# Performance work log

Measured on AMD Instinct MI355X. Metric: run time of the kernel, lower is better.

Reference implementation:

```python
import jax, jax.numpy as jnp
import numpy as np

NODE_DIM = 32
EDGE_DIM = 16
N_A = 1024
N_B = 1024
EDGE_IN = 2 * NODE_DIM + 2 * EDGE_DIM   # 96
NODE_IN = NODE_DIM + EDGE_DIM           # 48


def _linear_init(key, fan_in, fan_out):
    # torch nn.Linear default init: U(-1/sqrt(fan_in), 1/sqrt(fan_in))
    kw, kb = jax.random.split(key)
    bound = 1.0 / np.sqrt(fan_in)
    W = jax.random.uniform(kw, (fan_in, fan_out), jnp.float32, -bound, bound)
    b = jax.random.uniform(kb, (fan_out,), jnp.float32, -bound, bound)
    return W, b


def setup_inputs() -> dict:
    key = jax.random.key(0)
    ks = jax.random.split(key, 7)
    edge_embeds = jax.random.normal(ks[0], (N_A, N_B, 2 * EDGE_DIM), jnp.float32)
    nodes_a_embeds = jax.random.normal(ks[1], (N_A, NODE_DIM), jnp.float32)
    nodes_b_embeds = jax.random.normal(ks[2], (N_B, NODE_DIM), jnp.float32)
    We1, be1 = _linear_init(ks[3], EDGE_IN, EDGE_DIM)
    We2, be2 = _linear_init(ks[4], EDGE_DIM, EDGE_DIM)
    Wn1, bn1 = _linear_init(ks[5], NODE_IN, NODE_DIM)
    Wn2, bn2 = _linear_init(ks[6], NODE_DIM, NODE_DIM)
    return {
        "edge_embeds": edge_embeds,
        "nodes_a_embeds": nodes_a_embeds,
        "nodes_b_embeds": nodes_b_embeds,
        "We1": We1, "be1": be1, "We2": We2, "be2": be2,
        "Wn1": Wn1, "bn1": bn1, "Wn2": Wn2, "bn2": bn2,
    }


def _edge_mlp(x, We1, be1, We2, be2):
    h = jax.nn.relu(x @ We1 + be1)
    return jax.nn.relu(h @ We2 + be2)


def _node_mlp(x, Wn1, bn1, Wn2, bn2):
    h = jax.nn.relu(x @ Wn1 + bn1)
    return jax.nn.relu(h @ Wn2 + bn2)


def reference(edge_embeds, nodes_a_embeds, nodes_b_embeds,
              We1, be1, We2, be2, Wn1, bn1, Wn2, bn2):
    nA, nB, _ = edge_embeds.shape
    # edge update: broadcast node feats over the bipartite grid, concat, 2-layer MLP
    a_bcast = jnp.broadcast_to(nodes_a_embeds[:, None, :], (nA, nB, NODE_DIM))
    b_bcast = jnp.broadcast_to(nodes_b_embeds[None, :, :], (nA, nB, NODE_DIM))
    edge_in = jnp.concatenate([a_bcast, b_bcast, edge_embeds], axis=-1)  # (A,B,96)
    new_edges = _edge_mlp(edge_in, We1, be1, We2, be2)                   # (A,B,E)
    # node update: sum-aggregate messages, concat with node feats, 2-layer MLP
    msg_to_a = new_edges.sum(axis=1)  # (A,E)
    msg_to_b = new_edges.sum(axis=0)  # (B,E)
    new_a = _node_mlp(jnp.concatenate([nodes_a_embeds, msg_to_a], axis=-1), Wn1, bn1, Wn2, bn2)
    new_b = _node_mlp(jnp.concatenate([nodes_b_embeds, msg_to_b], axis=-1), Wn1, bn1, Wn2, bn2)
    return (new_edges, new_a, new_b)
```

## Files before the change

kernel.cpp:

```cpp
#include <hip/hip_runtime.h>
#include <hip/hip_bf16.h>

typedef float f32x4 __attribute__((ext_vector_type(4)));
typedef short s16x8 __attribute__((ext_vector_type(8)));

__device__ __forceinline__ unsigned short f2bf(float x) {
  return __bfloat16_as_ushort(__float2bfloat16(x));
}

__global__ void preab_kernel(const float* __restrict__ na, const float* __restrict__ nb,
                             const float* __restrict__ We1, const float* __restrict__ be1,
                             float* __restrict__ preA, float* __restrict__ preB) {
  int tid = blockIdx.x * blockDim.x + threadIdx.x;
  bool isB = tid >= 1024;
  int row = tid & 1023;
  const float* x = (isB ? nb : na) + row * 32;
  const float* W = We1 + (isB ? 32 * 16 : 0);
  float acc[16];
#pragma unroll
  for (int k = 0; k < 16; ++k) acc[k] = isB ? be1[k] : 0.f;
#pragma unroll
  for (int v = 0; v < 32; ++v) {
    float xv = x[v];
#pragma unroll
    for (int k = 0; k < 16; ++k) acc[k] += xv * W[v * 16 + k];
  }
  float* dst = (isB ? preB : preA) + row * 16;
#pragma unroll
  for (int q = 0; q < 4; ++q) {
    f32x4 o = {acc[q * 4], acc[q * 4 + 1], acc[q * 4 + 2], acc[q * 4 + 3]};
    *(f32x4*)&dst[q * 4] = o;
  }
}

__global__ __launch_bounds__(256, 4)
void edge_kernel(const float* __restrict__ E,
                 const float* __restrict__ We1,
                 const float* __restrict__ We2,
                 const float* __restrict__ be2,
                 const float* __restrict__ preA_g,
                 const float* __restrict__ preB_g,
                 float* __restrict__ outE,
                 float* __restrict__ msgA,
                 float* __restrict__ msgB) {
  __shared__ float sA[32 * 16];
  __shared__ float sB[32 * 20];
  __shared__ float sCS[4 * 512];

  const int t = threadIdx.x;
  const int bi = blockIdx.y, bj = blockIdx.x;

  if (t < 128) {
    int r = t >> 2, q = (t & 3) << 2;
    *(f32x4*)&sA[r * 16 + q] = *(const f32x4*)&preA_g[(bi * 32 + r) * 16 + q];
  } else {
    int tt = t - 128, r = tt >> 2, q = (tt & 3) << 2;
    *(f32x4*)&sB[r * 20 + q] = *(const f32x4*)&preB_g[(bj * 32 + r) * 16 + q];
  }

  const int w = t >> 6, lane = t & 63, G = lane >> 4, n = lane & 15;

  s16x8 a1, a2;
#pragma unroll
  for (int i2 = 0; i2 < 8; ++i2) {
    int k = G * 8 + i2;
    a1[i2] = (short)f2bf(We1[(64 + k) * 16 + n]);
    a2[i2] = (k < 16) ? (short)f2bf(We2[k * 16 + n]) : (short)0;
  }
  const f32x4 bq = *(const f32x4*)&be2[G * 4];

  __syncthreads();

  f32x4 cs0 = {0.f, 0.f, 0.f, 0.f}, cs1 = {0.f, 0.f, 0.f, 0.f};
  const f32x4 zero = {0.f, 0.f, 0.f, 0.f};

  for (int ii = 0; ii < 8; ++ii) {
    const int iloc = w * 8 + ii;
    const int i = bi * 32 + iloc;
    const f32x4 pA = *(const f32x4*)&sA[iloc * 16 + G * 4];
    f32x4 rs = {0.f, 0.f, 0.f, 0.f};
#pragma unroll
    for (int jg = 0; jg < 2; ++jg) {
      const int j = bj * 32 + jg * 16 + n;
      const float* ep = E + ((long)(i * 1024 + j) << 5) + G * 8;
      f32x4 e0 = __builtin_nontemporal_load((const f32x4*)ep);
      f32x4 e1 = __builtin_nontemporal_load((const f32x4*)(ep + 4));
      s16x8 bf;
      bf[0] = (short)f2bf(e0[0]); bf[1] = (short)f2bf(e0[1]);
      bf[2] = (short)f2bf(e0[2]); bf[3] = (short)f2bf(e0[3]);
      bf[4] = (short)f2bf(e1[0]); bf[5] = (short)f2bf(e1[1]);
      bf[6] = (short)f2bf(e1[2]); bf[7] = (short)f2bf(e1[3]);
      f32x4 d1 = __builtin_amdgcn_mfma_f32_16x16x32_bf16(a1, bf, zero, 0, 0, 0);
      const f32x4 pB = *(const f32x4*)&sB[(jg * 16 + n) * 20 + G * 4];
      float h0 = fmaxf(d1[0] + pA[0] + pB[0], 0.f);
      float h1 = fmaxf(d1[1] + pA[1] + pB[1], 0.f);
      float h2 = fmaxf(d1[2] + pA[2] + pB[2], 0.f);
      float h3 = fmaxf(d1[3] + pA[3] + pB[3], 0.f);
      unsigned p0 = (unsigned)f2bf(h0) | ((unsigned)f2bf(h1) << 16);
      unsigned p1 = (unsigned)f2bf(h2) | ((unsigned)f2bf(h3) << 16);
      int s0 = G * 32 + n;
      unsigned u0 = (unsigned)__shfl((int)p0, s0);
      unsigned u1 = (unsigned)__shfl((int)p1, s0);
      unsigned u2 = (unsigned)__shfl((int)p0, s0 + 16);
      unsigned u3 = (unsigned)__shfl((int)p1, s0 + 16);
      union { s16x8 v; unsigned u[4]; } b2;
      b2.u[0] = u0; b2.u[1] = u1; b2.u[2] = u2; b2.u[3] = u3;
      f32x4 d2 = __builtin_amdgcn_mfma_f32_16x16x32_bf16(a2, b2.v, zero, 0, 0, 0);
      f32x4 o;
      o[0] = fmaxf(d2[0] + bq[0], 0.f);
      o[1] = fmaxf(d2[1] + bq[1], 0.f);
      o[2] = fmaxf(d2[2] + bq[2], 0.f);
      o[3] = fmaxf(d2[3] + bq[3], 0.f);
      __builtin_nontemporal_store(o, (f32x4*)&outE[((long)(i * 1024 + j) << 4) + G * 4]);
      rs += o;
      if (jg == 0) cs0 += o; else cs1 += o;
    }
#pragma unroll
    for (int mask = 1; mask < 16; mask <<= 1) {
      rs[0] += __shfl_xor(rs[0], mask);
      rs[1] += __shfl_xor(rs[1], mask);
      rs[2] += __shfl_xor(rs[2], mask);
      rs[3] += __shfl_xor(rs[3], mask);
    }
    if (n < 4) {
      float val = (n == 0) ? rs[0] : (n == 1) ? rs[1] : (n == 2) ? rs[2] : rs[3];
      atomicAdd(&msgA[i * 16 + G * 4 + n], val);
    }
  }
  *(f32x4*)&sCS[w * 512 + n * 16 + G * 4] = cs0;
  *(f32x4*)&sCS[w * 512 + 256 + n * 16 + G * 4] = cs1;
  __syncthreads();
#pragma unroll
  for (int rep = 0; rep < 2; ++rep) {
    int idx = t + rep * 256;
    float s = sCS[idx] + sCS[512 + idx] + sCS[1024 + idx] + sCS[1536 + idx];
    int jg = idx >> 8, jl = (idx >> 4) & 15, c = idx & 15;
    atomicAdd(&msgB[(bj * 32 + jg * 16 + jl) * 16 + c], s);
  }
}

__global__ void node_kernel(const float* __restrict__ na, const float* __restrict__ nb,
                            const float* __restrict__ msgA, const float* __restrict__ msgB,
                            const float* __restrict__ Wn1, const float* __restrict__ bn1,
                            const float* __restrict__ Wn2, const float* __restrict__ bn2,
                            float* __restrict__ outA, float* __restrict__ outB) {
  int tid = blockIdx.x * blockDim.x + threadIdx.x;
  bool isB = tid >= 1024;
  int row = tid & 1023;
  const float* x0 = (isB ? nb : na) + row * 32;
  const float* m0 = (isB ? msgB : msgA) + row * 16;
  float h[32];
#pragma unroll
  for (int m = 0; m < 32; ++m) h[m] = bn1[m];
#pragma unroll 4
  for (int v = 0; v < 32; ++v) {
    float xv = x0[v];
#pragma unroll
    for (int m = 0; m < 32; ++m) h[m] += xv * Wn1[v * 32 + m];
  }
#pragma unroll 4
  for (int v = 0; v < 16; ++v) {
    float mv = m0[v];
#pragma unroll
    for (int m = 0; m < 32; ++m) h[m] += mv * Wn1[(32 + v) * 32 + m];
  }
#pragma unroll
  for (int m = 0; m < 32; ++m) h[m] = fmaxf(h[m], 0.f);
  float* dst = (isB ? outB : outA) + row * 32;
#pragma unroll 4
  for (int c = 0; c < 32; ++c) {
    float s = bn2[c];
#pragma unroll
    for (int m = 0; m < 32; ++m) s += h[m] * Wn2[m * 32 + c];
    dst[c] = fmaxf(s, 0.f);
  }
}

extern "C" void kernel_launch(void* const* d_in, const int* in_sizes, int n_in,
                              void* d_out, int out_size, void* d_ws, size_t ws_size,
                              hipStream_t stream) {
  const float* E   = (const float*)d_in[0];
  const float* na  = (const float*)d_in[1];
  const float* nb  = (const float*)d_in[2];
  const float* We1 = (const float*)d_in[3];
  const float* be1 = (const float*)d_in[4];
  const float* We2 = (const float*)d_in[5];
  const float* be2 = (const float*)d_in[6];
  const float* Wn1 = (const float*)d_in[7];
  const float* bn1 = (const float*)d_in[8];
  const float* Wn2 = (const float*)d_in[9];
  const float* bn2 = (const float*)d_in[10];

  float* out  = (float*)d_out;
  float* outE = out;
  float* outA = out + 16777216;
  float* outB = outA + 32768;

  float* ws   = (float*)d_ws;
  float* preA = ws;
  float* preB = ws + 16384;
  float* msgA = ws + 32768;
  float* msgB = ws + 49152;

  hipMemsetAsync(msgA, 0, 2 * 16384 * sizeof(float), stream);
  preab_kernel<<<dim3(8), dim3(256), 0, stream>>>(na, nb, We1, be1, preA, preB);
  edge_kernel<<<dim3(32, 32), dim3(256), 0, stream>>>(E, We1, We2, be2, preA, preB,
                                                      outE, msgA, msgB);
  node_kernel<<<dim3(8), dim3(256), 0, stream>>>(na, nb, msgA, msgB,
                                                 Wn1, bn1, Wn2, bn2, outA, outB);
}
```

Before: 261.7 us.

## Fuse node pre-projection into edge kernel and replace atomics with partial-sum buffers

Folds the separate pre-projection kernel into the edge kernel, where each block computes its own 32-row A/B projections. Global atomics for the message sums are replaced by per-block partial writes that the node kernel reduces, which also removes the memset. The second edge layer now uses a 16x16x16 MFMA with no cross-lane shuffles, and the edge loads for both column groups are issued up front. In exchange, each block recomputes small projections, and the node kernel must read 32 partials per row.

```diff
diff --git a/kernel.cpp b/kernel.cpp
--- a/kernel.cpp
+++ b/kernel.cpp
@@ -3,46 +3,33 @@
 
 typedef float f32x4 __attribute__((ext_vector_type(4)));
 typedef short s16x8 __attribute__((ext_vector_type(8)));
+typedef short s16x4 __attribute__((ext_vector_type(4)));
 
 __device__ __forceinline__ unsigned short f2bf(float x) {
   return __bfloat16_as_ushort(__float2bfloat16(x));
 }
 
-__global__ void preab_kernel(const float* __restrict__ na, const float* __restrict__ nb,
-                             const float* __restrict__ We1, const float* __restrict__ be1,
-                             float* __restrict__ preA, float* __restrict__ preB) {
-  int tid = blockIdx.x * blockDim.x + threadIdx.x;
-  bool isB = tid >= 1024;
-  int row = tid & 1023;
-  const float* x = (isB ? nb : na) + row * 32;
-  const float* W = We1 + (isB ? 32 * 16 : 0);
-  float acc[16];
-#pragma unroll
-  for (int k = 0; k < 16; ++k) acc[k] = isB ? be1[k] : 0.f;
-#pragma unroll
-  for (int v = 0; v < 32; ++v) {
-    float xv = x[v];
-#pragma unroll
-    for (int k = 0; k < 16; ++k) acc[k] += xv * W[v * 16 + k];
-  }
-  float* dst = (isB ? preB : preA) + row * 16;
-#pragma unroll
-  for (int q = 0; q < 4; ++q) {
-    f32x4 o = {acc[q * 4], acc[q * 4 + 1], acc[q * 4 + 2], acc[q * 4 + 3]};
-    *(f32x4*)&dst[q * 4] = o;
-  }
+__device__ __forceinline__ f32x4 mfma16x16x16_bf16(s16x4 a, s16x4 b, f32x4 c) {
+#if __has_builtin(__builtin_amdgcn_mfma_f32_16x16x16bf16_1k)
+  return __builtin_amdgcn_mfma_f32_16x16x16bf16_1k(a, b, c, 0, 0, 0);
+#else
+  f32x4 d;
+  asm("v_mfma_f32_16x16x16_bf16 %0, %1, %2, %3" : "=v"(d) : "v"(a), "v"(b), "v"(c));
+  return d;
+#endif
 }
 
 __global__ __launch_bounds__(256, 4)
 void edge_kernel(const float* __restrict__ E,
+                 const float* __restrict__ na,
+                 const float* __restrict__ nb,
                  const float* __restrict__ We1,
+                 const float* __restrict__ be1,
                  const float* __restrict__ We2,
                  const float* __restrict__ be2,
-                 const float* __restrict__ preA_g,
-                 const float* __restrict__ preB_g,
                  float* __restrict__ outE,
-                 float* __restrict__ msgA,
-                 float* __restrict__ msgB) {
+                 float* __restrict__ rowP,
+                 float* __restrict__ colP) {
   __shared__ float sA[32 * 16];
   __shared__ float sB[32 * 20];
   __shared__ float sCS[4 * 512];
@@ -50,62 +37,73 @@
   const int t = threadIdx.x;
   const int bi = blockIdx.y, bj = blockIdx.x;
 
-  if (t < 128) {
-    int r = t >> 2, q = (t & 3) << 2;
-    *(f32x4*)&sA[r * 16 + q] = *(const f32x4*)&preA_g[(bi * 32 + r) * 16 + q];
-  } else {
-    int tt = t - 128, r = tt >> 2, q = (tt & 3) << 2;
-    *(f32x4*)&sB[r * 20 + q] = *(const f32x4*)&preB_g[(bj * 32 + r) * 16 + q];
+  {
+    const bool half = t >= 128;
+    const int tt = t & 127, r = tt >> 2, qs = (tt & 3) << 2;
+    const float* x = (half ? nb : na) + (half ? bj : bi) * 32 * 32 + r * 32;
+    const float* W = We1 + (half ? 32 * 16 : 0) + qs;
+    f32x4 acc;
+    if (half) acc = *(const f32x4*)&be1[qs];
+    else { acc[0] = acc[1] = acc[2] = acc[3] = 0.f; }
+#pragma unroll 8
+    for (int v = 0; v < 32; ++v) {
+      float xv = x[v];
+      f32x4 wv = *(const f32x4*)&W[v * 16];
+      acc[0] += xv * wv[0]; acc[1] += xv * wv[1];
+      acc[2] += xv * wv[2]; acc[3] += xv * wv[3];
+    }
+    if (half) *(f32x4*)&sB[r * 20 + qs] = acc;
+    else      *(f32x4*)&sA[r * 16 + qs] = acc;
   }
 
   const int w = t >> 6, lane = t & 63, G = lane >> 4, n = lane & 15;
 
-  s16x8 a1, a2;
-#pragma unroll
-  for (int i2 = 0; i2 < 8; ++i2) {
-    int k = G * 8 + i2;
-    a1[i2] = (short)f2bf(We1[(64 + k) * 16 + n]);
-    a2[i2] = (k < 16) ? (short)f2bf(We2[k * 16 + n]) : (short)0;
-  }
+  s16x8 a1;
+  s16x4 a2;
+#pragma unroll
+  for (int i2 = 0; i2 < 8; ++i2) a1[i2] = (short)f2bf(We1[(64 + G * 8 + i2) * 16 + n]);
+#pragma unroll
+  for (int i2 = 0; i2 < 4; ++i2) a2[i2] = (short)f2bf(We2[(G * 4 + i2) * 16 + n]);
   const f32x4 bq = *(const f32x4*)&be2[G * 4];
 
   __syncthreads();
 
   f32x4 cs0 = {0.f, 0.f, 0.f, 0.f}, cs1 = {0.f, 0.f, 0.f, 0.f};
   const f32x4 zero = {0.f, 0.f, 0.f, 0.f};
-
+  const f32x4 pB0 = *(const f32x4*)&sB[n * 20 + G * 4];
+  const f32x4 pB1 = *(const f32x4*)&sB[(16 + n) * 20 + G * 4];
+
+#pragma unroll 2
   for (int ii = 0; ii < 8; ++ii) {
     const int iloc = w * 8 + ii;
     const int i = bi * 32 + iloc;
+    const float* ep = E + ((long)(i * 1024 + bj * 32 + n) << 5) + G * 8;
+    f32x4 e00 = __builtin_nontemporal_load((const f32x4*)ep);
+    f32x4 e01 = __builtin_nontemporal_load((const f32x4*)(ep + 4));
+    f32x4 e10 = __builtin_nontemporal_load((const f32x4*)(ep + 512));
+    f32x4 e11 = __builtin_nontemporal_load((const f32x4*)(ep + 516));
     const f32x4 pA = *(const f32x4*)&sA[iloc * 16 + G * 4];
     f32x4 rs = {0.f, 0.f, 0.f, 0.f};
 #pragma unroll
     for (int jg = 0; jg < 2; ++jg) {
+      const f32x4 ea = jg ? e10 : e00;
+      const f32x4 eb = jg ? e11 : e01;
+      const f32x4 pB = jg ? pB1 : pB0;
       const int j = bj * 32 + jg * 16 + n;
-      const float* ep = E + ((long)(i * 1024 + j) << 5) + G * 8;
-      f32x4 e0 = __builtin_nontemporal_load((const f32x4*)ep);
-      f32x4 e1 = __builtin_nontemporal_load((const f32x4*)(ep + 4));
       s16x8 bf;
-      bf[0] = (short)f2bf(e0[0]); bf[1] = (short)f2bf(e0[1]);
-      bf[2] = (short)f2bf(e0[2]); bf[3] = (short)f2bf(e0[3]);
-      bf[4] = (short)f2bf(e1[0]); bf[5] = (short)f2bf(e1[1]);
-      bf[6] = (short)f2bf(e1[2]); bf[7] = (short)f2bf(e1[3]);
+      bf[0] = (short)f2bf(ea[0]); bf[1] = (short)f2bf(ea[1]);
+      bf[2] = (short)f2bf(ea[2]); bf[3] = (short)f2bf(ea[3]);
+      bf[4] = (short)f2bf(eb[0]); bf[5] = (short)f2bf(eb[1]);
+      bf[6] = (short)f2bf(eb[2]); bf[7] = (short)f2bf(eb[3]);
       f32x4 d1 = __builtin_amdgcn_mfma_f32_16x16x32_bf16(a1, bf, zero, 0, 0, 0);
-      const f32x4 pB = *(const f32x4*)&sB[(jg * 16 + n) * 20 + G * 4];
       float h0 = fmaxf(d1[0] + pA[0] + pB[0], 0.f);
       float h1 = fmaxf(d1[1] + pA[1] + pB[1], 0.f);
       float h2 = fmaxf(d1[2] + pA[2] + pB[2], 0.f);
       float h3 = fmaxf(d1[3] + pA[3] + pB[3], 0.f);
-      unsigned p0 = (unsigned)f2bf(h0) | ((unsigned)f2bf(h1) << 16);
-      unsigned p1 = (unsigned)f2bf(h2) | ((unsigned)f2bf(h3) << 16);
-      int s0 = G * 32 + n;
-      unsigned u0 = (unsigned)__shfl((int)p0, s0);
-      unsigned u1 = (unsigned)__shfl((int)p1, s0);
-      unsigned u2 = (unsigned)__shfl((int)p0, s0 + 16);
-      unsigned u3 = (unsigned)__shfl((int)p1, s0 + 16);
-      union { s16x8 v; unsigned u[4]; } b2;
-      b2.u[0] = u0; b2.u[1] = u1; b2.u[2] = u2; b2.u[3] = u3;
-      f32x4 d2 = __builtin_amdgcn_mfma_f32_16x16x32_bf16(a2, b2.v, zero, 0, 0, 0);
+      s16x4 b2;
+      b2[0] = (short)f2bf(h0); b2[1] = (short)f2bf(h1);
+      b2[2] = (short)f2bf(h2); b2[3] = (short)f2bf(h3);
+      f32x4 d2 = mfma16x16x16_bf16(a2, b2, zero);
       f32x4 o;
       o[0] = fmaxf(d2[0] + bq[0], 0.f);
       o[1] = fmaxf(d2[1] + bq[1], 0.f);
@@ -124,7 +122,7 @@
     }
     if (n < 4) {
       float val = (n == 0) ? rs[0] : (n == 1) ? rs[1] : (n == 2) ? rs[2] : rs[3];
-      atomicAdd(&msgA[i * 16 + G * 4 + n], val);
+      rowP[bj * 16384 + i * 16 + G * 4 + n] = val;
     }
   }
   *(f32x4*)&sCS[w * 512 + n * 16 + G * 4] = cs0;
@@ -134,13 +132,13 @@
   for (int rep = 0; rep < 2; ++rep) {
     int idx = t + rep * 256;
     float s = sCS[idx] + sCS[512 + idx] + sCS[1024 + idx] + sCS[1536 + idx];
-    int jg = idx >> 8, jl = (idx >> 4) & 15, c = idx & 15;
-    atomicAdd(&msgB[(bj * 32 + jg * 16 + jl) * 16 + c], s);
+    int jl = idx >> 4, c = idx & 15;
+    colP[bi * 16384 + (bj * 32 + jl) * 16 + c] = s;
   }
 }
 
 __global__ void node_kernel(const float* __restrict__ na, const float* __restrict__ nb,
-                            const float* __restrict__ msgA, const float* __restrict__ msgB,
+                            const float* __restrict__ rowP, const float* __restrict__ colP,
                             const float* __restrict__ Wn1, const float* __restrict__ bn1,
                             const float* __restrict__ Wn2, const float* __restrict__ bn2,
                             float* __restrict__ outA, float* __restrict__ outB) {
@@ -148,7 +146,19 @@
   bool isB = tid >= 1024;
   int row = tid & 1023;
   const float* x0 = (isB ? nb : na) + row * 32;
-  const float* m0 = (isB ? msgB : msgA) + row * 16;
+  const float* P = (isB ? colP : rowP) + row * 16;
+  f32x4 m0 = {0.f,0.f,0.f,0.f}, m1 = m0, m2 = m0, m3 = m0;
+#pragma unroll 4
+  for (int b = 0; b < 32; ++b) {
+    const float* p = P + b * 16384;
+    m0 += *(const f32x4*)&p[0];
+    m1 += *(const f32x4*)&p[4];
+    m2 += *(const f32x4*)&p[8];
+    m3 += *(const f32x4*)&p[12];
+  }
+  union { f32x4 v[4]; float f[16]; } mm;
+  mm.v[0] = m0; mm.v[1] = m1; mm.v[2] = m2; mm.v[3] = m3;
+
   float h[32];
 #pragma unroll
   for (int m = 0; m < 32; ++m) h[m] = bn1[m];
@@ -160,7 +170,7 @@
   }
 #pragma unroll 4
   for (int v = 0; v < 16; ++v) {
-    float mv = m0[v];
+    float mv = mm.f[v];
 #pragma unroll
     for (int m = 0; m < 32; ++m) h[m] += mv * Wn1[(32 + v) * 32 + m];
   }
@@ -197,15 +207,11 @@
   float* outB = outA + 32768;
 
   float* ws   = (float*)d_ws;
-  float* preA = ws;
-  float* preB = ws + 16384;
-  float* msgA = ws + 32768;
-  float* msgB = ws + 49152;
-
-  hipMemsetAsync(msgA, 0, 2 * 16384 * sizeof(float), stream);
-  preab_kernel<<<dim3(8), dim3(256), 0, stream>>>(na, nb, We1, be1, preA, preB);
-  edge_kernel<<<dim3(32, 32), dim3(256), 0, stream>>>(E, We1, We2, be2, preA, preB,
-                                                      outE, msgA, msgB);
-  node_kernel<<<dim3(8), dim3(256), 0, stream>>>(na, nb, msgA, msgB,
+  float* rowP = ws;
+  float* colP = ws + 524288;
+
+  edge_kernel<<<dim3(32, 32), dim3(256), 0, stream>>>(E, na, nb, We1, be1, We2, be2,
+                                                      outE, rowP, colP);
+  node_kernel<<<dim3(8), dim3(256), 0, stream>>>(na, nb, rowP, colP,
                                                  Wn1, bn1, Wn2, bn2, outA, outB);
 }
```

Result: no change. 258.0 us (-1.4%).
